# Kernel tuning notes

Measured on AMD Instinct MI355X. Metric: run time of the kernel, lower is better.

The kernel has to match this reference:

```python
import jax, jax.numpy as jnp
import numpy as np

B, D, E, N = 2048, 4096, 512, 8192
BN_EPS = 1e-5
COS_EPS = 1e-8


def setup_inputs() -> dict:
    key = jax.random.key(0)
    k1, k2, k3, k4, k5 = jax.random.split(key, 5)
    vf = jax.random.normal(k1, (B, D), dtype=jnp.float32)
    p_wfs = jax.random.normal(k2, (B, D), dtype=jnp.float32)
    n_wfs = jax.random.normal(k3, (N, E), dtype=jnp.float32)
    # BatchNorm1d(4096) affine params (default init gamma=1, beta=0; use random-ish gamma for generality)
    gamma = jnp.ones((D,), dtype=jnp.float32)
    beta = jnp.zeros((D,), dtype=jnp.float32)
    # Linear(D -> E)
    lim = 1.0 / np.sqrt(D)
    W = jax.random.uniform(k4, (E, D), dtype=jnp.float32, minval=-lim, maxval=lim)
    b = jax.random.uniform(k5, (E,), dtype=jnp.float32, minval=-lim, maxval=lim)
    return {"vf": vf, "p_wfs": p_wfs, "n_wfs": n_wfs, "gamma": gamma, "beta": beta, "W": W, "b": b}


def _row_normalize(x, eps=COS_EPS):
    nrm = jnp.sqrt(jnp.sum(x * x, axis=-1, keepdims=True))
    return x / jnp.maximum(nrm, eps)


def reference(vf, p_wfs, n_wfs, gamma, beta, W, b):
    # BatchNorm1d in training mode: batch mean / biased variance over the batch dim
    mean = jnp.mean(vf, axis=0)
    var = jnp.mean((vf - mean) ** 2, axis=0)
    vfn = (vf - mean) * (gamma / jnp.sqrt(var + BN_EPS)) + beta  # [B, D]

    # Linear + ReLU embedding
    emb = jax.nn.relu(vfn @ W.T + b)  # [B, E]

    # p_e: row-wise cosine(normed vf, p_wfs) -> [B]
    p_e = jnp.sum(_row_normalize(vfn) * _row_normalize(p_wfs), axis=-1)

    # n_e: cosine(emb[v], n_wfs[n]) for all v,n -> one normalized GEMM [B, N]
    n_e = _row_normalize(emb) @ _row_normalize(n_wfs).T

    n_neg = n_wfs.shape[0]
    n_e_stack = n_e.reshape(-1, 1)                      # [B*N, 1]
    p_e_stack = jnp.repeat(p_e, n_neg).reshape(-1, 1)   # [B*N, 1], p_e[v] repeated N times
    return (n_e_stack, p_e_stack)
```

## Files before the change

### kernel.cpp

```cpp
#include <hip/hip_runtime.h>
#include <stdint.h>
#include <stddef.h>

#define B_ 2048
#define D_ 4096
#define E_ 512
#define N_ 8192
#define SPLITK 4

typedef unsigned short ushort_t;
typedef __attribute__((ext_vector_type(8))) short short8;
typedef __attribute__((ext_vector_type(4))) float floatx4;
typedef __attribute__((ext_vector_type(4))) unsigned short ushort4_t;

__device__ __forceinline__ void async_load16(const void* g, void* l) {
  __builtin_amdgcn_global_load_lds((__attribute__((address_space(1))) void*)(g),
                                   (__attribute__((address_space(3))) void*)(l), 16, 0, 0);
}

__device__ __forceinline__ ushort_t f2bf(float f) {
  unsigned int u = __float_as_uint(f);
  unsigned int r = (u + 0x7fffu + ((u >> 16) & 1u)) >> 16;
  return (ushort_t)r;
}
__device__ __forceinline__ float bf2f(ushort_t h) {
  return __uint_as_float(((unsigned int)h) << 16);
}

__global__ __launch_bounds__(256) void bn_partial(const float* __restrict__ vf,
                                                  float* __restrict__ psum,
                                                  float* __restrict__ psq) {
  int d4 = blockIdx.x * 256 + threadIdx.x;
  int chunk = blockIdx.y;
  floatx4 s = {0.f, 0.f, 0.f, 0.f}, q = {0.f, 0.f, 0.f, 0.f};
  int r0 = chunk * 32;
  for (int r = r0; r < r0 + 32; ++r) {
    floatx4 v = ((const floatx4*)(vf + (size_t)r * D_))[d4];
    s += v; q += v * v;
  }
  ((floatx4*)(psum + (size_t)chunk * D_))[d4] = s;
  ((floatx4*)(psq  + (size_t)chunk * D_))[d4] = q;
}

__global__ __launch_bounds__(256) void prep_all(const float* __restrict__ psum,
                                                const float* __restrict__ psq,
                                                const float* __restrict__ gamma,
                                                const float* __restrict__ beta,
                                                const float* __restrict__ W,
                                                const float* __restrict__ nw,
                                                float* __restrict__ scale,
                                                float* __restrict__ shift,
                                                ushort_t* __restrict__ wb,
                                                ushort_t* __restrict__ nwb,
                                                float* __restrict__ inv_nw) {
  int bid = blockIdx.x;
  if (bid < 4) {
    int d4 = bid * 256 + threadIdx.x;
    floatx4 s = {0.f, 0.f, 0.f, 0.f}, q = {0.f, 0.f, 0.f, 0.f};
    for (int c = 0; c < 64; ++c) {
      s += ((const floatx4*)(psum + (size_t)c * D_))[d4];
      q += ((const floatx4*)(psq  + (size_t)c * D_))[d4];
    }
    floatx4 g = ((const floatx4*)gamma)[d4];
    floatx4 bt = ((const floatx4*)beta)[d4];
    floatx4 sc, sh;
#pragma unroll
    for (int j = 0; j < 4; ++j) {
      float mean = s[j] * (1.0f / B_);
      float var  = q[j] * (1.0f / B_) - mean * mean;
      float scj  = g[j] * rsqrtf(var + 1e-5f);
      sc[j] = scj;
      sh[j] = bt[j] - mean * scj;
    }
    ((floatx4*)scale)[d4] = sc;
    ((floatx4*)shift)[d4] = sh;
  } else if (bid < 2052) {
    size_t i = ((size_t)(bid - 4) * 256 + threadIdx.x) * 4;
    floatx4 x = *(const floatx4*)(W + i);
    ushort4_t o;
#pragma unroll
    for (int j = 0; j < 4; ++j) o[j] = f2bf(x[j]);
    *(ushort4_t*)(wb + i) = o;
  } else {
    int wv = threadIdx.x >> 6, l = threadIdx.x & 63;
    int n = (bid - 2052) * 4 + wv;
    const floatx4* src = (const floatx4*)(nw + (size_t)n * E_);
    ushort4_t* dst = (ushort4_t*)(nwb + (size_t)n * E_);
    float s = 0.f;
#pragma unroll
    for (int k = 0; k < 2; ++k) {
      floatx4 x = src[l + 64 * k];
      ushort4_t o;
#pragma unroll
      for (int j = 0; j < 4; ++j) { o[j] = f2bf(x[j]); s += x[j] * x[j]; }
      dst[l + 64 * k] = o;
    }
    for (int off = 32; off; off >>= 1) s += __shfl_down(s, off);
    if (l == 0) inv_nw[n] = 1.f / fmaxf(sqrtf(s), 1e-8f);
  }
}

__global__ __launch_bounds__(256) void pe_cast(const float* __restrict__ vf,
                                               const float* __restrict__ p,
                                               const float* __restrict__ scale,
                                               const float* __restrict__ shift,
                                               ushort_t* __restrict__ vfn,
                                               float* __restrict__ pe) {
  int wv = threadIdx.x >> 6, l = threadIdx.x & 63;
  int v = blockIdx.x * 4 + wv;
  const floatx4* vf4 = (const floatx4*)(vf + (size_t)v * D_);
  const floatx4* p4  = (const floatx4*)(p  + (size_t)v * D_);
  const floatx4* sc4 = (const floatx4*)scale;
  const floatx4* sh4 = (const floatx4*)shift;
  ushort_t* vrow = vfn + (size_t)v * D_;
  float sd = 0.f, sa = 0.f, sb = 0.f;
#pragma unroll 4
  for (int k = 0; k < 16; ++k) {
    int i = l + 64 * k;
    floatx4 x = vf4[i], y = p4[i], s = sc4[i], t = sh4[i];
    ushort4_t o;
#pragma unroll
    for (int j = 0; j < 4; ++j) {
      float xn = x[j] * s[j] + t[j];
      o[j] = f2bf(xn);
      sd += xn * y[j]; sa += xn * xn; sb += y[j] * y[j];
    }
    *(ushort4_t*)(vrow + i * 4) = o;
  }
  for (int off = 32; off; off >>= 1) {
    sd += __shfl_down(sd, off); sa += __shfl_down(sa, off); sb += __shfl_down(sb, off);
  }
  if (l == 0) {
    float na = fmaxf(sqrtf(sa), 1e-8f), nb = fmaxf(sqrtf(sb), 1e-8f);
    pe[v] = sd / (na * nb);
  }
}

template <int BM, int BN, int BK, int WCOLS, int MT, int NT>
__device__ __forceinline__ void gemm_core(const ushort_t* __restrict__ A,
                                          const ushort_t* __restrict__ Bt, int K,
                                          int kb, int ke, int bm0, int bn0,
                                          ushort_t* As, ushort_t* Bs,
                                          floatx4 (&acc)[MT][NT]) {
  const int tid = threadIdx.x, w = tid >> 6, l = tid & 63;
  constexpr int ISS_A = BM * BK / 2048;
  constexpr int ISS_B = BN * BK / 2048;
  const int wr = w / WCOLS, wc = w % WCOLS;
  const int m16 = l & 15, q = l >> 4;

  for (int k0 = kb; k0 < ke; k0 += BK) {
#pragma unroll
    for (int i = 0; i < ISS_A; ++i) {
      int e = i * 2048 + tid * 8;
      int row = e / BK, col = e % BK;
      async_load16(A + (size_t)(bm0 + row) * K + (k0 + col), &As[i * 2048 + w * 512]);
    }
#pragma unroll
    for (int i = 0; i < ISS_B; ++i) {
      int e = i * 2048 + tid * 8;
      int row = e / BK, col = e % BK;
      async_load16(Bt + (size_t)(bn0 + row) * K + (k0 + col), &Bs[i * 2048 + w * 512]);
    }
    __syncthreads();
#pragma unroll
    for (int kc = 0; kc < BK / 32; ++kc) {
      short8 af[MT], bf[NT];
#pragma unroll
      for (int i = 0; i < MT; ++i)
        af[i] = *(const short8*)&As[(wr * (MT * 16) + i * 16 + m16) * BK + kc * 32 + q * 8];
#pragma unroll
      for (int j = 0; j < NT; ++j)
        bf[j] = *(const short8*)&Bs[(wc * (NT * 16) + j * 16 + m16) * BK + kc * 32 + q * 8];
#pragma unroll
      for (int i = 0; i < MT; ++i)
#pragma unroll
        for (int j = 0; j < NT; ++j)
          acc[i][j] = __builtin_amdgcn_mfma_f32_16x16x32_bf16(af[i], bf[j], acc[i][j], 0, 0, 0);
    }
    __syncthreads();
  }
}

__global__ __launch_bounds__(256, 2) void gemm1_splitk(const ushort_t* __restrict__ A,
                                                       const ushort_t* __restrict__ Bt,
                                                       float* __restrict__ partial) {
  __shared__ __align__(16) ushort_t As[128 * 64];
  __shared__ __align__(16) ushort_t Bs[64 * 64];
  floatx4 acc[4][2] = {};
  int bm0 = blockIdx.y * 128, bn0 = blockIdx.x * 64, s = blockIdx.z;
  int kb = s * (D_ / SPLITK);
  gemm_core<128, 64, 64, 2, 4, 2>(A, Bt, D_, kb, kb + D_ / SPLITK, bm0, bn0, As, Bs, acc);
  int tid = threadIdx.x, w = tid >> 6, l = tid & 63, m16 = l & 15, q = l >> 4;
  int wr = w >> 1, wc = w & 1;
  float* out = partial + (size_t)s * B_ * E_;
#pragma unroll
  for (int i = 0; i < 4; ++i)
#pragma unroll
    for (int j = 0; j < 2; ++j) {
      int col = bn0 + wc * 32 + j * 16 + m16;
#pragma unroll
      for (int r = 0; r < 4; ++r) {
        int row = bm0 + wr * 64 + i * 16 + q * 4 + r;
        out[(size_t)row * E_ + col] = acc[i][j][r];
      }
    }
}

__global__ __launch_bounds__(256) void gemm1_reduce(const float* __restrict__ partial,
                                                    const float* __restrict__ bias,
                                                    ushort_t* __restrict__ emb,
                                                    float* __restrict__ inv_emb) {
  int wv = threadIdx.x >> 6, l = threadIdx.x & 63;
  int row = blockIdx.x * 4 + wv;
  float sumsq = 0.f;
#pragma unroll
  for (int k = 0; k < 2; ++k) {
    int i = l + 64 * k;
    floatx4 v = {0.f, 0.f, 0.f, 0.f};
#pragma unroll
    for (int s = 0; s < SPLITK; ++s)
      v += ((const floatx4*)(partial + (size_t)s * B_ * E_ + (size_t)row * E_))[i];
    floatx4 bb = ((const floatx4*)bias)[i];
    ushort4_t o;
#pragma unroll
    for (int j = 0; j < 4; ++j) {
      float f = fmaxf(v[j] + bb[j], 0.f);
      o[j] = f2bf(f);
      float fb = bf2f(o[j]);
      sumsq += fb * fb;
    }
    ((ushort4_t*)(emb + (size_t)row * E_))[i] = o;
  }
  for (int off = 32; off; off >>= 1) sumsq += __shfl_down(sumsq, off);
  if (l == 0) inv_emb[row] = 1.f / fmaxf(sqrtf(sumsq), 1e-8f);
}

__global__ __launch_bounds__(256, 2) void gemm2_kernel(const ushort_t* __restrict__ A,
                                                       const ushort_t* __restrict__ Bt,
                                                       const float* __restrict__ inv_a,
                                                       const float* __restrict__ inv_b,
                                                       const float* __restrict__ pe,
                                                       float* __restrict__ out) {
  __shared__ __align__(16) ushort_t As[128 * 64];
  __shared__ __align__(16) ushort_t Bs[128 * 64];
  floatx4 acc[4][4] = {};
  const int tid = threadIdx.x, w = tid >> 6, l = tid & 63;
  const int m16 = l & 15, q = l >> 4;
  const int wr = w >> 1, wc = w & 1;
  const int bm0 = blockIdx.y * 128, bn0 = blockIdx.x * 128;

  float pv[4][4];
#pragma unroll
  for (int i = 0; i < 4; ++i)
#pragma unroll
    for (int r = 0; r < 4; ++r)
      pv[i][r] = pe[bm0 + wr * 64 + i * 16 + q * 4 + r];
  float* out2lane = out + (size_t)B_ * N_ + bn0 + wc * 64 + m16;

#pragma unroll
  for (int it = 0; it < E_ / 64; ++it) {
    int k0 = it * 64;
#pragma unroll
    for (int i = 0; i < 4; ++i) {
      int e = i * 2048 + tid * 8;
      async_load16(A + (size_t)(bm0 + e / 64) * E_ + (k0 + e % 64), &As[i * 2048 + w * 512]);
    }
#pragma unroll
    for (int i = 0; i < 4; ++i) {
      int e = i * 2048 + tid * 8;
      async_load16(Bt + (size_t)(bn0 + e / 64) * E_ + (k0 + e % 64), &Bs[i * 2048 + w * 512]);
    }
    __syncthreads();
#pragma unroll
    for (int t = 0; t < 8; ++t) {
      int idx = it * 8 + t;
      int i = idx >> 4, r = (idx >> 2) & 3, j = idx & 3;
      int row = bm0 + wr * 64 + i * 16 + q * 4 + r;
      out2lane[(size_t)row * N_ + j * 16] = pv[i][r];
    }
#pragma unroll
    for (int kc = 0; kc < 2; ++kc) {
      short8 af[4], bf[4];
#pragma unroll
      for (int i = 0; i < 4; ++i)
        af[i] = *(const short8*)&As[(wr * 64 + i * 16 + m16) * 64 + kc * 32 + q * 8];
#pragma unroll
      for (int j = 0; j < 4; ++j)
        bf[j] = *(const short8*)&Bs[(wc * 64 + j * 16 + m16) * 64 + kc * 32 + q * 8];
#pragma unroll
      for (int i = 0; i < 4; ++i)
#pragma unroll
        for (int j = 0; j < 4; ++j)
          acc[i][j] = __builtin_amdgcn_mfma_f32_16x16x32_bf16(af[i], bf[j], acc[i][j], 0, 0, 0);
    }
    __syncthreads();
  }

  float ibv[4];
#pragma unroll
  for (int j = 0; j < 4; ++j) ibv[j] = inv_b[bn0 + wc * 64 + j * 16 + m16];
#pragma unroll
  for (int i = 0; i < 4; ++i)
#pragma unroll
    for (int r = 0; r < 4; ++r) {
      int row = bm0 + wr * 64 + i * 16 + q * 4 + r;
      float ia = inv_a[row];
      size_t base = (size_t)row * N_ + bn0 + wc * 64 + m16;
#pragma unroll
      for (int j = 0; j < 4; ++j)
        out[base + j * 16] = acc[i][j][r] * ia * ibv[j];
    }
}

extern "C" void kernel_launch(void* const* d_in, const int* in_sizes, int n_in,
                              void* d_out, int out_size, void* d_ws, size_t ws_size,
                              hipStream_t stream) {
  (void)in_sizes; (void)n_in; (void)out_size; (void)ws_size;
  const float* vf    = (const float*)d_in[0];
  const float* p_wfs = (const float*)d_in[1];
  const float* n_wfs = (const float*)d_in[2];
  const float* gamma = (const float*)d_in[3];
  const float* beta  = (const float*)d_in[4];
  const float* W     = (const float*)d_in[5];
  const float* bias  = (const float*)d_in[6];
  float* out = (float*)d_out;

  char* ws = (char*)d_ws;
  float* psum    = (float*)ws;  ws += (size_t)64 * D_ * 4;
  float* psq     = (float*)ws;  ws += (size_t)64 * D_ * 4;
  float* scale   = (float*)ws;  ws += (size_t)D_ * 4;
  float* shift   = (float*)ws;  ws += (size_t)D_ * 4;
  float* pe      = (float*)ws;  ws += (size_t)B_ * 4;
  float* inv_nw  = (float*)ws;  ws += (size_t)N_ * 4;
  float* inv_emb = (float*)ws;  ws += (size_t)B_ * 4;
  float* partial = (float*)ws;  ws += (size_t)SPLITK * B_ * E_ * 4;
  ushort_t* vfn  = (ushort_t*)ws;  ws += (size_t)B_ * D_ * 2;
  ushort_t* wb   = (ushort_t*)ws;  ws += (size_t)E_ * D_ * 2;
  ushort_t* nwb  = (ushort_t*)ws;  ws += (size_t)N_ * E_ * 2;
  ushort_t* emb  = (ushort_t*)ws;  ws += (size_t)B_ * E_ * 2;

  bn_partial<<<dim3(D_ / 1024, 64), 256, 0, stream>>>(vf, psum, psq);
  prep_all<<<4 + 2048 + N_ / 4, 256, 0, stream>>>(psum, psq, gamma, beta, W, n_wfs,
                                                  scale, shift, wb, nwb, inv_nw);
  pe_cast<<<B_ / 4, 256, 0, stream>>>(vf, p_wfs, scale, shift, vfn, pe);
  gemm1_splitk<<<dim3(E_ / 64, B_ / 128, SPLITK), 256, 0, stream>>>(vfn, wb, partial);
  gemm1_reduce<<<B_ / 4, 256, 0, stream>>>(partial, bias, emb, inv_emb);
  gemm2_kernel<<<dim3(N_ / 128, B_ / 128), 256, 0, stream>>>(emb, nwb, inv_emb, inv_nw, pe, out);
}
```

Measured before the change: 272.2 us.

## Restructure gemm2 to stage full-K B tile in LDS and stream A from global

gemm2 now uses a 128x64 output tile per block. The entire 64x512 slice of n_wfs is loaded into LDS once, and each wave reads its 32 rows of A directly from global memory as it walks K. This removes the per-K-step barriers and LDS staging of A, and doubles the grid size. In exchange it needs 64KB of LDS per block, which may limit occupancy, and A reads go straight to global/cache with no reuse across waves.

```diff
diff --git a/kernel.cpp b/kernel.cpp
--- a/kernel.cpp
+++ b/kernel.cpp
@@ -241,71 +241,63 @@
                                                        const float* __restrict__ inv_b,
                                                        const float* __restrict__ pe,
                                                        float* __restrict__ out) {
-  __shared__ __align__(16) ushort_t As[128 * 64];
-  __shared__ __align__(16) ushort_t Bs[128 * 64];
-  floatx4 acc[4][4] = {};
+  __shared__ __align__(16) ushort_t Bs[64 * 512];
   const int tid = threadIdx.x, w = tid >> 6, l = tid & 63;
   const int m16 = l & 15, q = l >> 4;
-  const int wr = w >> 1, wc = w & 1;
-  const int bm0 = blockIdx.y * 128, bn0 = blockIdx.x * 128;
-
-  float pv[4][4];
-#pragma unroll
-  for (int i = 0; i < 4; ++i)
+  const int bm0 = blockIdx.y * 128, bn0 = blockIdx.x * 64;
+
+#pragma unroll
+  for (int r = 0; r < 16; ++r) {
+    int row = w * 16 + r;
+    async_load16(Bt + (size_t)(bn0 + row) * E_ + l * 8, &Bs[row * 512 + l * 8]);
+  }
+
+  const int arow = bm0 + w * 32;
+  float pv[2][4];
+#pragma unroll
+  for (int i = 0; i < 2; ++i)
 #pragma unroll
     for (int r = 0; r < 4; ++r)
-      pv[i][r] = pe[bm0 + wr * 64 + i * 16 + q * 4 + r];
-  float* out2lane = out + (size_t)B_ * N_ + bn0 + wc * 64 + m16;
-
-#pragma unroll
-  for (int it = 0; it < E_ / 64; ++it) {
-    int k0 = it * 64;
-#pragma unroll
-    for (int i = 0; i < 4; ++i) {
-      int e = i * 2048 + tid * 8;
-      async_load16(A + (size_t)(bm0 + e / 64) * E_ + (k0 + e % 64), &As[i * 2048 + w * 512]);
-    }
-#pragma unroll
-    for (int i = 0; i < 4; ++i) {
-      int e = i * 2048 + tid * 8;
-      async_load16(Bt + (size_t)(bn0 + e / 64) * E_ + (k0 + e % 64), &Bs[i * 2048 + w * 512]);
-    }
-    __syncthreads();
-#pragma unroll
-    for (int t = 0; t < 8; ++t) {
-      int idx = it * 8 + t;
-      int i = idx >> 4, r = (idx >> 2) & 3, j = idx & 3;
-      int row = bm0 + wr * 64 + i * 16 + q * 4 + r;
+      pv[i][r] = pe[arow + i * 16 + q * 4 + r];
+  float* out2lane = out + (size_t)B_ * N_ + bn0 + m16;
+
+  floatx4 acc[2][4] = {};
+  __syncthreads();
+
+#pragma unroll
+  for (int ks = 0; ks < 16; ++ks) {
+    int k0 = ks * 32 + q * 8;
+    short8 af[2], bf[4];
+#pragma unroll
+    for (int i = 0; i < 2; ++i)
+      af[i] = *(const short8*)(A + (size_t)(arow + i * 16 + m16) * E_ + k0);
+#pragma unroll
+    for (int j = 0; j < 4; ++j)
+      bf[j] = *(const short8*)&Bs[(j * 16 + m16) * 512 + k0];
+#pragma unroll
+    for (int t = 0; t < 2; ++t) {
+      int id = ks * 2 + t;
+      int i = id >> 4, r = (id >> 2) & 3, j = id & 3;
+      int row = arow + i * 16 + q * 4 + r;
       out2lane[(size_t)row * N_ + j * 16] = pv[i][r];
     }
 #pragma unroll
-    for (int kc = 0; kc < 2; ++kc) {
-      short8 af[4], bf[4];
-#pragma unroll
-      for (int i = 0; i < 4; ++i)
-        af[i] = *(const short8*)&As[(wr * 64 + i * 16 + m16) * 64 + kc * 32 + q * 8];
+    for (int i = 0; i < 2; ++i)
 #pragma unroll
       for (int j = 0; j < 4; ++j)
-        bf[j] = *(const short8*)&Bs[(wc * 64 + j * 16 + m16) * 64 + kc * 32 + q * 8];
-#pragma unroll
-      for (int i = 0; i < 4; ++i)
-#pragma unroll
-        for (int j = 0; j < 4; ++j)
-          acc[i][j] = __builtin_amdgcn_mfma_f32_16x16x32_bf16(af[i], bf[j], acc[i][j], 0, 0, 0);
-    }
-    __syncthreads();
+        acc[i][j] = __builtin_amdgcn_mfma_f32_16x16x32_bf16(af[i], bf[j], acc[i][j], 0, 0, 0);
   }
 
   float ibv[4];
 #pragma unroll
-  for (int j = 0; j < 4; ++j) ibv[j] = inv_b[bn0 + wc * 64 + j * 16 + m16];
-#pragma unroll
-  for (int i = 0; i < 4; ++i)
+  for (int j = 0; j < 4; ++j) ibv[j] = inv_b[bn0 + j * 16 + m16];
+#pragma unroll
+  for (int i = 0; i < 2; ++i)
 #pragma unroll
     for (int r = 0; r < 4; ++r) {
-      int row = bm0 + wr * 64 + i * 16 + q * 4 + r;
+      int row = arow + i * 16 + q * 4 + r;
       float ia = inv_a[row];
-      size_t base = (size_t)row * N_ + bn0 + wc * 64 + m16;
+      size_t base = (size_t)row * N_ + bn0 + m16;
 #pragma unroll
       for (int j = 0; j < 4; ++j)
         out[base + j * 16] = acc[i][j][r] * ia * ibv[j];
@@ -345,5 +337,5 @@
   pe_cast<<<B_ / 4, 256, 0, stream>>>(vf, p_wfs, scale, shift, vfn, pe);
   gemm1_splitk<<<dim3(E_ / 64, B_ / 128, SPLITK), 256, 0, stream>>>(vfn, wb, partial);
   gemm1_reduce<<<B_ / 4, 256, 0, stream>>>(partial, bias, emb, inv_emb);
-  gemm2_kernel<<<dim3(N_ / 128, B_ / 128), 256, 0, stream>>>(emb, nwb, inv_emb, inv_nw, pe, out);
-}
+  gemm2_kernel<<<dim3(N_ / 64, B_ / 128), 256, 0, stream>>>(emb, nwb, inv_emb, inv_nw, pe, out);
+}
```

After: 288.9 us. 1.06x slower.
